# Optimization experiments

Hardware: AMD Instinct MI355X
Metric: run time of the kernel (lower is better)

Reference implementation:

```python
import jax, jax.numpy as jnp
import numpy as np

K = 7
SIGMA = 1.0
NUM_CLASSES = 17


def setup_inputs() -> dict:
    key = jax.random.key(0)
    k1, k2, k3 = jax.random.split(key, 3)
    B, C, N = 4, NUM_CLASSES, 4096
    logits = jax.random.normal(k1, (B, C, N), dtype=jnp.float32)
    labels = jax.random.randint(k2, (B, N), 0, NUM_CLASSES, dtype=jnp.int32)
    ins_T = jax.random.normal(k3, (B * N, NUM_CLASSES, NUM_CLASSES), dtype=jnp.float32)
    return {"logits": logits, "labels": labels, "ins_T": ins_T}


def reference(logits, labels, ins_T):
    B, C, N = logits.shape
    k = K
    x = jnp.transpose(logits, (0, 2, 1))  # [B, N, C]

    # Pairwise squared distances [B, N, N] and (k+1)-NN (smallest dists)
    sq = jnp.sum(x * x, axis=-1)  # [B, N]
    dists = sq[:, :, None] + sq[:, None, :] - 2.0 * jnp.einsum('bnc,bmc->bnm', x, x)
    _, idx = jax.lax.top_k(-dists, k + 1)  # smallest distances first
    idx = idx[:, :, 1:]  # drop self -> [B, N, k]

    flat = x.reshape(B * N, C)                 # [BN, C]
    labf = labels.reshape(-1)                  # [BN]
    idxf = (idx + jnp.arange(B)[:, None, None] * N).reshape(B * N, k)  # [BN, k]

    neigh_logits = flat[idxf]                          # [BN, k, C]
    neigh_labels = labf[idxf]                          # [BN, k]
    neigh_T = ins_T[idxf].reshape(B * N, k, -1)        # [BN, k, C*C]

    # distance map: +1 same label, -1 different, weighted by RBF affinity
    dmap = jnp.where(neigh_labels == labf[:, None], 1.0, -1.0)
    eij = jnp.exp(-jnp.sum((flat[:, None, :] - neigh_logits) ** 2, axis=2)
                  / (2.0 * SIGMA ** 2))
    dmap = jax.lax.stop_gradient(dmap * eij)  # detached in original

    T_dist = jnp.sum((ins_T.reshape(B * N, 1, -1) - neigh_T) ** 2, axis=2)  # [BN, k]
    return jnp.mean(dmap * T_dist)
```

## Files before the change

### kernel.cpp

```cpp
#include <hip/hip_runtime.h>

#define BB 4
#define CC 17
#define NN 4096
#define KN 7
#define NPTS (BB*NN)
#define PAIRS (NPTS*KN)
#define TT (CC*CC)
#define FINF 3.4e38f
#define WSL 4
#define CSL 1024
#define NTW (CSL/16)
#define SCAP 128

typedef float f32x4 __attribute__((ext_vector_type(4)));
typedef short short8 __attribute__((ext_vector_type(8)));

__device__ __forceinline__ unsigned int rne_bf16(float x) {
    unsigned int u = __float_as_uint(x);
    return (u + 0x7FFFu + ((u >> 16) & 1u)) >> 16;
}

__device__ __forceinline__ bool lexless(float ad, int ai, float bd, int bi) {
    return (ad < bd) || (ad == bd && ai < bi);
}

__global__ __launch_bounds__(256) void prep_kernel(const float* __restrict__ logits,
                                                   float* __restrict__ xs,
                                                   unsigned short* __restrict__ xb,
                                                   float* __restrict__ sq) {
    int i = blockIdx.x * blockDim.x + threadIdx.x;
    if (i >= NPTS) return;
    int b = i >> 12;
    int n = i & (NN - 1);
    const float* base = logits + (size_t)b * CC * NN + n;
    float v[24];
    float s = 0.f;
#pragma unroll
    for (int c = 0; c < CC; ++c) { v[c] = base[(size_t)c * NN]; s = fmaf(v[c], v[c], s); }
#pragma unroll
    for (int c = CC; c < 24; ++c) v[c] = 0.f;
    float4* dst = (float4*)(xs + (size_t)i * 24);
#pragma unroll
    for (int q = 0; q < 6; ++q)
        dst[q] = make_float4(v[4*q], v[4*q+1], v[4*q+2], v[4*q+3]);
    sq[i] = s;
    unsigned int w[16];
#pragma unroll
    for (int t = 0; t < 16; ++t) {
        unsigned int u0 = (2*t   < CC) ? rne_bf16(v[2*t])   : 0u;
        unsigned int u1 = (2*t+1 < CC) ? rne_bf16(v[2*t+1]) : 0u;
        w[t] = u0 | (u1 << 16);
    }
    uint4* xd = (uint4*)(xb + (size_t)i * 32);
#pragma unroll
    for (int q = 0; q < 4; ++q)
        xd[q] = make_uint4(w[4*q], w[4*q+1], w[4*q+2], w[4*q+3]);
}

__global__ __launch_bounds__(256) void knn_kernel(const unsigned short* __restrict__ xb,
                                                  const float* __restrict__ sq,
                                                  const float* __restrict__ xs,
                                                  int* __restrict__ nidx) {
    int wid   = threadIdx.x >> 6;
    int lane  = threadIdx.x & 63;
    int strip = blockIdx.x;
    int b     = strip >> 8;
    int cb    = b * NN + wid * CSL;
    int col   = lane & 15;
    int grp   = lane >> 4;
    int k0    = grp * 8;

    __shared__ float thr_lds[WSL][16];
    __shared__ int   scnt[16];
    __shared__ int   slist[16][SCAP];
    if (threadIdx.x < 16) scnt[threadIdx.x] = 0;

    short8 A = *reinterpret_cast<const short8*>(xb + (size_t)(strip * 16 + col) * 32 + k0);
    const unsigned short* bp = xb + (size_t)(cb + col) * 32 + k0;
    const float* sp = sq + cb + col;
    f32x4 z = {0.f, 0.f, 0.f, 0.f};

    float t1[4], t2[4];
#pragma unroll
    for (int j = 0; j < 4; ++j) { t1[j] = FINF; t2[j] = FINF; }
#pragma unroll 8
    for (int t = 0; t < NTW; ++t) {
        short8 Bf = *reinterpret_cast<const short8*>(bp + (size_t)t * 512);
        float sqv = sp[t * 16];
        f32x4 acc = __builtin_amdgcn_mfma_f32_16x16x32_bf16(A, Bf, z, 0, 0, 0);
#pragma unroll
        for (int j = 0; j < 4; ++j) {
            float r  = fmaf(-2.f, acc[j], sqv);
            float hi = fmaxf(t1[j], r);
            t1[j] = fminf(t1[j], r);
            t2[j] = fminf(t2[j], hi);
        }
    }
#pragma unroll
    for (int j = 0; j < 4; ++j) {
        float a = t1[j], b2 = t2[j], m8 = FINF;
#pragma unroll
        for (int r = 0; r < 8; ++r) {
            float d = a;
            d = fminf(d, __shfl_xor(d, 1));
            d = fminf(d, __shfl_xor(d, 2));
            d = fminf(d, __shfl_xor(d, 4));
            d = fminf(d, __shfl_xor(d, 8));
            m8 = d;
            if (a == d) { a = b2; b2 = FINF; }
        }
        if (col == 0) thr_lds[wid][grp * 4 + j] = m8;
    }
    __syncthreads();

    float tj[4];
#pragma unroll
    for (int j = 0; j < 4; ++j) {
        int rr = grp * 4 + j;
        float m = fminf(fminf(thr_lds[0][rr], thr_lds[1][rr]),
                        fminf(thr_lds[2][rr], thr_lds[3][rr]));
        tj[j] = m + 0.5f + 0.005f * fabsf(m);
    }
    unsigned long long msk[4] = {0ull, 0ull, 0ull, 0ull};
#pragma unroll 4
    for (int t = 0; t < NTW; ++t) {
        short8 Bf = *reinterpret_cast<const short8*>(bp + (size_t)t * 512);
        float sqv = sp[t * 16];
        f32x4 acc = __builtin_amdgcn_mfma_f32_16x16x32_bf16(A, Bf, z, 0, 0, 0);
#pragma unroll
        for (int j = 0; j < 4; ++j) {
            float r = fmaf(-2.f, acc[j], sqv);
            msk[j] |= (r < tj[j]) ? (1ull << t) : 0ull;
        }
    }
#pragma unroll
    for (int j = 0; j < 4; ++j) {
        unsigned long long w = msk[j];
        int rloc = grp * 4 + j;
        while (w) {
            int t = __builtin_ctzll(w); w &= w - 1;
            int slot = atomicAdd(&scnt[rloc], 1);
            if (slot < SCAP) slist[rloc][slot] = cb + t * 16 + col;
        }
    }
    __syncthreads();

#pragma unroll 1
    for (int rr4 = 0; rr4 < 4; ++rr4) {
        int rloc = wid * 4 + rr4;
        int rowg = strip * 16 + rloc;
        int n = scnt[rloc]; n = (n > SCAP) ? SCAP : n;

        const float4* qp = (const float4*)(xs + (size_t)rowg * 24);
        float qv[20];
#pragma unroll
        for (int c = 0; c < 5; ++c) {
            float4 t = qp[c];
            qv[4*c] = t.x; qv[4*c+1] = t.y; qv[4*c+2] = t.z; qv[4*c+3] = t.w;
        }

        float d1 = FINF, d2 = FINF;
        int   i1 = 0x40000000 + lane, i2 = 0x44000000 + lane;
#pragma unroll
        for (int h = 0; h < 2; ++h) {
            int slot = lane + 64 * h;
            if (slot < n) {
                int g = slist[rloc][slot];
                const float4* xp = (const float4*)(xs + (size_t)g * 24);
                float dot = 0.f;
#pragma unroll
                for (int c = 0; c < 5; ++c) {
                    float4 xv = xp[c];
                    dot = fmaf(qv[4*c+0], xv.x, dot);
                    dot = fmaf(qv[4*c+1], xv.y, dot);
                    dot = fmaf(qv[4*c+2], xv.z, dot);
                    dot = fmaf(qv[4*c+3], xv.w, dot);
                }
                float r = fmaf(-2.f, dot, sq[g]);
                if (g == rowg) r = FINF;
                if (h == 0) { d1 = r; i1 = g; } else { d2 = r; i2 = g; }
            }
        }
        if (lexless(d2, i2, d1, i1)) {
            float td = d1; d1 = d2; d2 = td;
            int   ti = i1; i1 = i2; i2 = ti;
        }

#pragma unroll
        for (int r = 0; r < KN; ++r) {
            float g = d1; int gi = i1;
#pragma unroll
            for (int off = 32; off >= 1; off >>= 1) {
                float od = __shfl_xor(g, off);
                int   oi = __shfl_xor(gi, off);
                if (lexless(od, oi, g, gi)) { g = od; gi = oi; }
            }
            if (lane == 0) nidx[(size_t)rowg * KN + r] = gi;
            if (i1 == gi) {
                d1 = d2; i1 = i2;
                d2 = FINF; i2 = 0x48000000 + lane * 8 + r;
            }
        }
    }
}

__global__ __launch_bounds__(256) void pair_kernel(const float* __restrict__ xs,
                                                   const int* __restrict__ labels,
                                                   const float* __restrict__ insT,
                                                   const int* __restrict__ nidx,
                                                   double* __restrict__ partials) {
    int wid  = threadIdx.x >> 6;
    int lane = threadIdx.x & 63;
    int row  = blockIdx.x * 4 + wid;
    int li   = labels[row];

    const float* Ti = insT + (size_t)row * TT;
    float tiv[5];
#pragma unroll
    for (int q = 0; q < 5; ++q) {
        int e = lane + 64 * q;
        tiv[q] = (e < TT) ? Ti[e] : 0.f;
    }
    float xi = (lane < 20) ? xs[(size_t)row * 24 + lane] : 0.f;

    double acc = 0.0;
#pragma unroll 1
    for (int kk = 0; kk < KN; ++kk) {
        int j = nidx[(size_t)row * KN + kk];
        const float* Tj = insT + (size_t)j * TT;
        float td = 0.f;
#pragma unroll
        for (int q = 0; q < 5; ++q) {
            int e = lane + 64 * q;
            if (e < TT) {
                float df = tiv[q] - Tj[e];
                td = fmaf(df, df, td);
            }
        }
        float dp = 0.f;
        if (lane < 20) {
            float df = xi - xs[(size_t)j * 24 + lane];
            dp = df * df;
        }
#pragma unroll
        for (int off = 32; off >= 1; off >>= 1) {
            td += __shfl_xor(td, off);
            dp += __shfl_xor(dp, off);
        }
        if (lane == 0) {
            float eij = expf(-0.5f * dp);
            float sgn = (labels[j] == li) ? eij : -eij;
            acc += (double)sgn * (double)td;
        }
    }
    __shared__ double wsum[4];
    if (lane == 0) wsum[wid] = acc;
    __syncthreads();
    if (threadIdx.x == 0)
        partials[blockIdx.x] = wsum[0] + wsum[1] + wsum[2] + wsum[3];
}

__global__ __launch_bounds__(1024) void finalize_kernel(const double* __restrict__ partials,
                                                        int nparts, float* __restrict__ out) {
    __shared__ double red[1024];
    int t = threadIdx.x;
    double s = 0.0;
    for (int q = t; q < nparts; q += 1024) s += partials[q];
    red[t] = s;
    __syncthreads();
    for (int sft = 512; sft > 0; sft >>= 1) {
        if (t < sft) red[t] += red[t + sft];
        __syncthreads();
    }
    if (t == 0) out[0] = (float)(red[0] / (double)PAIRS);
}

extern "C" void kernel_launch(void* const* d_in, const int* in_sizes, int n_in,
                              void* d_out, int out_size, void* d_ws, size_t ws_size,
                              hipStream_t stream) {
    const float* logits = (const float*)d_in[0];
    const int*   labels = (const int*)d_in[1];
    const float* insT   = (const float*)d_in[2];
    float* out = (float*)d_out;

    char* ws = (char*)d_ws;
    const size_t o_part = 0;
    const size_t o_nidx = 32768;
    const size_t o_sq   = o_nidx + 458752;
    const size_t o_xs   = o_sq + 65536;
    const size_t o_xb   = o_xs + 1572864;

    double*         partials = (double*)(ws + o_part);
    int*            nidx     = (int*)(ws + o_nidx);
    float*          sq       = (float*)(ws + o_sq);
    float*          xs       = (float*)(ws + o_xs);
    unsigned short* xb       = (unsigned short*)(ws + o_xb);

    hipLaunchKernelGGL(prep_kernel, dim3(NPTS / 256), dim3(256), 0, stream,
                       logits, xs, xb, sq);
    hipLaunchKernelGGL(knn_kernel, dim3(NPTS / 16), dim3(256), 0, stream,
                       xb, sq, xs, nidx);
    hipLaunchKernelGGL(pair_kernel, dim3(NPTS / 4), dim3(256), 0, stream,
                       xs, labels, insT, nidx, partials);
    hipLaunchKernelGGL(finalize_kernel, dim3(1), dim3(1024), 0, stream,
                       partials, NPTS / 4, out);
}
```

Baseline: 101.7 us.

## Split KNN over eight waves and replace shuffle top-k with LDS rerank

The KNN kernel now uses 512-thread blocks with eight waves, each scanning 512 columns. The first-pass threshold is simplified to a rank count over the per-column minima, which drops the second-min tracking. Candidates are pushed with LDS atomics directly during the second pass. The exact rerank is spread over 32 threads per row into LDS, then 16 threads each select their row's top-7 with a serial insertion sort over 96 slots. This aims to cut per-wave serial work and the wave-wide shuffle reductions. The risks are a looser threshold that could overflow the smaller 96-entry candidate cap, and a serial selection tail.

Measured after the change: 136.1 us. 33.9% more time.

```diff
diff --git a/kernel.cpp b/kernel.cpp
--- a/kernel.cpp
+++ b/kernel.cpp
@@ -8,10 +8,10 @@
 #define PAIRS (NPTS*KN)
 #define TT (CC*CC)
 #define FINF 3.4e38f
-#define WSL 4
-#define CSL 1024
-#define NTW (CSL/16)
-#define SCAP 128
+#define NWV 8
+#define CSW 512
+#define NTW (CSW/16)
+#define SCAP 96
 
 typedef float f32x4 __attribute__((ext_vector_type(4)));
 typedef short short8 __attribute__((ext_vector_type(8)));
@@ -58,59 +58,57 @@
         xd[q] = make_uint4(w[4*q], w[4*q+1], w[4*q+2], w[4*q+3]);
 }
 
-__global__ __launch_bounds__(256) void knn_kernel(const unsigned short* __restrict__ xb,
+__global__ __launch_bounds__(512) void knn_kernel(const unsigned short* __restrict__ xb,
                                                   const float* __restrict__ sq,
                                                   const float* __restrict__ xs,
                                                   int* __restrict__ nidx) {
-    int wid   = threadIdx.x >> 6;
-    int lane  = threadIdx.x & 63;
+    int tid   = threadIdx.x;
+    int wid   = tid >> 6;
+    int lane  = tid & 63;
     int strip = blockIdx.x;
     int b     = strip >> 8;
-    int cb    = b * NN + wid * CSL;
+    int cb    = b * NN + wid * CSW;
     int col   = lane & 15;
     int grp   = lane >> 4;
     int k0    = grp * 8;
 
-    __shared__ float thr_lds[WSL][16];
+    __shared__ float thr_lds[NWV][16];
     __shared__ int   scnt[16];
     __shared__ int   slist[16][SCAP];
-    if (threadIdx.x < 16) scnt[threadIdx.x] = 0;
+    __shared__ float srank[16][SCAP];
+    if (tid < 16) scnt[tid] = 0;
 
     short8 A = *reinterpret_cast<const short8*>(xb + (size_t)(strip * 16 + col) * 32 + k0);
     const unsigned short* bp = xb + (size_t)(cb + col) * 32 + k0;
     const float* sp = sq + cb + col;
     f32x4 z = {0.f, 0.f, 0.f, 0.f};
 
-    float t1[4], t2[4];
-#pragma unroll
-    for (int j = 0; j < 4; ++j) { t1[j] = FINF; t2[j] = FINF; }
+    float t1[4] = {FINF, FINF, FINF, FINF};
 #pragma unroll 8
     for (int t = 0; t < NTW; ++t) {
         short8 Bf = *reinterpret_cast<const short8*>(bp + (size_t)t * 512);
         float sqv = sp[t * 16];
         f32x4 acc = __builtin_amdgcn_mfma_f32_16x16x32_bf16(A, Bf, z, 0, 0, 0);
 #pragma unroll
-        for (int j = 0; j < 4; ++j) {
-            float r  = fmaf(-2.f, acc[j], sqv);
-            float hi = fmaxf(t1[j], r);
-            t1[j] = fminf(t1[j], r);
-            t2[j] = fminf(t2[j], hi);
-        }
-    }
+        for (int j = 0; j < 4; ++j)
+            t1[j] = fminf(t1[j], fmaf(-2.f, acc[j], sqv));
+    }
+
 #pragma unroll
     for (int j = 0; j < 4; ++j) {
-        float a = t1[j], b2 = t2[j], m8 = FINF;
-#pragma unroll
-        for (int r = 0; r < 8; ++r) {
-            float d = a;
-            d = fminf(d, __shfl_xor(d, 1));
-            d = fminf(d, __shfl_xor(d, 2));
-            d = fminf(d, __shfl_xor(d, 4));
-            d = fminf(d, __shfl_xor(d, 8));
-            m8 = d;
-            if (a == d) { a = b2; b2 = FINF; }
-        }
-        if (col == 0) thr_lds[wid][grp * 4 + j] = m8;
+        float v = t1[j];
+        int cnt = 0;
+#pragma unroll
+        for (int m = 1; m < 16; ++m) {
+            float o = __shfl_xor(v, m);
+            cnt += (o < v) ? 1 : 0;
+        }
+        float bv = (cnt <= 7) ? v : -FINF;
+        bv = fmaxf(bv, __shfl_xor(bv, 1));
+        bv = fmaxf(bv, __shfl_xor(bv, 2));
+        bv = fmaxf(bv, __shfl_xor(bv, 4));
+        bv = fmaxf(bv, __shfl_xor(bv, 8));
+        if (col == 0) thr_lds[wid][grp * 4 + j] = bv;
     }
     __syncthreads();
 
@@ -118,11 +116,11 @@
 #pragma unroll
     for (int j = 0; j < 4; ++j) {
         int rr = grp * 4 + j;
-        float m = fminf(fminf(thr_lds[0][rr], thr_lds[1][rr]),
-                        fminf(thr_lds[2][rr], thr_lds[3][rr]));
+        float m = FINF;
+#pragma unroll
+        for (int w = 0; w < NWV; ++w) m = fminf(m, thr_lds[w][rr]);
         tj[j] = m + 0.5f + 0.005f * fabsf(m);
     }
-    unsigned long long msk[4] = {0ull, 0ull, 0ull, 0ull};
 #pragma unroll 4
     for (int t = 0; t < NTW; ++t) {
         short8 Bf = *reinterpret_cast<const short8*>(bp + (size_t)t * 512);
@@ -131,27 +129,19 @@
 #pragma unroll
         for (int j = 0; j < 4; ++j) {
             float r = fmaf(-2.f, acc[j], sqv);
-            msk[j] |= (r < tj[j]) ? (1ull << t) : 0ull;
-        }
-    }
-#pragma unroll
-    for (int j = 0; j < 4; ++j) {
-        unsigned long long w = msk[j];
-        int rloc = grp * 4 + j;
-        while (w) {
-            int t = __builtin_ctzll(w); w &= w - 1;
-            int slot = atomicAdd(&scnt[rloc], 1);
-            if (slot < SCAP) slist[rloc][slot] = cb + t * 16 + col;
-        }
-    }
-    __syncthreads();
-
-#pragma unroll 1
-    for (int rr4 = 0; rr4 < 4; ++rr4) {
-        int rloc = wid * 4 + rr4;
-        int rowg = strip * 16 + rloc;
-        int n = scnt[rloc]; n = (n > SCAP) ? SCAP : n;
-
+            if (r < tj[j]) {
+                int rloc = grp * 4 + j;
+                int slot = atomicAdd(&scnt[rloc], 1);
+                if (slot < SCAP) slist[rloc][slot] = cb + t * 16 + col;
+            }
+        }
+    }
+    __syncthreads();
+
+    {
+        int row  = tid >> 5;
+        int rowg = strip * 16 + row;
+        int cnt  = scnt[row]; cnt = (cnt > SCAP) ? SCAP : cnt;
         const float4* qp = (const float4*)(xs + (size_t)rowg * 24);
         float qv[20];
 #pragma unroll
@@ -159,14 +149,12 @@
             float4 t = qp[c];
             qv[4*c] = t.x; qv[4*c+1] = t.y; qv[4*c+2] = t.z; qv[4*c+3] = t.w;
         }
-
-        float d1 = FINF, d2 = FINF;
-        int   i1 = 0x40000000 + lane, i2 = 0x44000000 + lane;
-#pragma unroll
-        for (int h = 0; h < 2; ++h) {
-            int slot = lane + 64 * h;
-            if (slot < n) {
-                int g = slist[rloc][slot];
+#pragma unroll
+        for (int h = 0; h < 3; ++h) {
+            int slot = (tid & 31) + 32 * h;
+            float r = FINF;
+            if (slot < cnt) {
+                int g = slist[row][slot];
                 const float4* xp = (const float4*)(xs + (size_t)g * 24);
                 float dot = 0.f;
 #pragma unroll
@@ -177,31 +165,38 @@
                     dot = fmaf(qv[4*c+2], xv.z, dot);
                     dot = fmaf(qv[4*c+3], xv.w, dot);
                 }
-                float r = fmaf(-2.f, dot, sq[g]);
+                r = fmaf(-2.f, dot, sq[g]);
                 if (g == rowg) r = FINF;
-                if (h == 0) { d1 = r; i1 = g; } else { d2 = r; i2 = g; }
             }
-        }
-        if (lexless(d2, i2, d1, i1)) {
-            float td = d1; d1 = d2; d2 = td;
-            int   ti = i1; i1 = i2; i2 = ti;
-        }
-
-#pragma unroll
-        for (int r = 0; r < KN; ++r) {
-            float g = d1; int gi = i1;
-#pragma unroll
-            for (int off = 32; off >= 1; off >>= 1) {
-                float od = __shfl_xor(g, off);
-                int   oi = __shfl_xor(gi, off);
-                if (lexless(od, oi, g, gi)) { g = od; gi = oi; }
+            srank[row][slot] = r;
+        }
+    }
+    __syncthreads();
+
+    if (tid < 16) {
+        int row  = tid;
+        int rowg = strip * 16 + row;
+        float bd[KN]; int bi[KN];
+#pragma unroll
+        for (int k = 0; k < KN; ++k) { bd[k] = FINF; bi[k] = 0x60000000 + row * 8 + k; }
+#pragma unroll 4
+        for (int s = 0; s < SCAP; ++s) {
+            float r = srank[row][s];
+            int   g = slist[row][s];
+            if (lexless(r, g, bd[KN-1], bi[KN-1])) {
+                bd[KN-1] = r; bi[KN-1] = g;
+#pragma unroll
+                for (int k = KN - 1; k >= 1; --k) {
+                    if (lexless(bd[k], bi[k], bd[k-1], bi[k-1])) {
+                        float td = bd[k]; bd[k] = bd[k-1]; bd[k-1] = td;
+                        int   ti = bi[k]; bi[k] = bi[k-1]; bi[k-1] = ti;
+                    }
+                }
             }
-            if (lane == 0) nidx[(size_t)rowg * KN + r] = gi;
-            if (i1 == gi) {
-                d1 = d2; i1 = i2;
-                d2 = FINF; i2 = 0x48000000 + lane * 8 + r;
-            }
-        }
+        }
+#pragma unroll
+        for (int k = 0; k < KN; ++k)
+            nidx[(size_t)rowg * KN + k] = bi[k];
     }
 }
 
@@ -299,7 +294,7 @@
 
     hipLaunchKernelGGL(prep_kernel, dim3(NPTS / 256), dim3(256), 0, stream,
                        logits, xs, xb, sq);
-    hipLaunchKernelGGL(knn_kernel, dim3(NPTS / 16), dim3(256), 0, stream,
+    hipLaunchKernelGGL(knn_kernel, dim3(NPTS / 16), dim3(512), 0, stream,
                        xb, sq, xs, nidx);
     hipLaunchKernelGGL(pair_kernel, dim3(NPTS / 4), dim3(256), 0, stream,
                        xs, labels, insT, nidx, partials);
```
